# Kernel tuning notes

Measured on AMD Instinct MI355X. Metric: run time of the kernel, lower is better.

Reference implementation:

```python
import jax, jax.numpy as jnp
import numpy as np

THRESHOLD = 0.5
TEMPERATURE = 4.0
LOG_CLAMP = -100.0  # torch BCELoss clamps log terms at -100

B, C, K = 131072, 128, 64


def setup_inputs() -> dict:
    key = jax.random.key(0)
    k1, k2, k3, k4, k5 = jax.random.split(key, 5)
    # sigmoid-like probabilities in (0, 1)
    output = jax.random.uniform(k1, (B, C), dtype=jnp.float32)
    output_consistency = jax.random.uniform(k2, (B, C), dtype=jnp.float32)
    label = jax.random.uniform(k3, (B, C), dtype=jnp.float32)
    class_idx = jnp.sort(jax.random.randint(k4, (K,), 0, C)).astype(jnp.int64)
    batch_mask = jax.random.randint(k5, (B,), 0, 2).astype(bool)
    return {
        "output": output,
        "output_consistency": output_consistency,
        "label": label,
        "class_idx": class_idx,
        "batch_mask": batch_mask,
    }


def _clamped_log(x):
    return jnp.maximum(jnp.log(x), LOG_CLAMP)


def reference(output, output_consistency, label, class_idx, batch_mask):
    # gather the class columns of interest: [B, K]
    o = output[:, class_idx]
    oc = output_consistency[:, class_idx]
    y = label[:, class_idx]

    # sharpened pseudo-label (branch on threshold, fused via where)
    sharp = jnp.where(o > THRESHOLD,
                      o + (1.0 - o) / TEMPERATURE,
                      o - o / TEMPERATURE)

    # per-element BCE (torch BCELoss semantics with log clamp)
    bce = -(y * _clamped_log(o) + (1.0 - y) * _clamped_log(1.0 - o))
    pseudo = (o - sharp) ** 2          # F.mse_loss on scalars
    consistency = (oc - sharp) ** 2

    per_elem = bce + pseudo + consistency            # [B, K]
    row_mask = batch_mask.astype(per_elem.dtype)     # [B]
    total = jnp.sum(per_elem * row_mask[:, None])
    cnt = jnp.sum(row_mask) * per_elem.shape[1]
    return total / cnt
```

## Files before the change

### kernel.cpp

```cpp
#include <hip/hip_runtime.h>

#define BLOCK  256
#define B_ROWS 131072
#define C_COLS 128
#define K_SEL  64
#define TOTAL_VEC (B_ROWS * C_COLS / 4)
#define GRID (TOTAL_VEC / BLOCK)


__global__ __launch_bounds__(BLOCK) void semi_loss_main(
    const float* __restrict__ out,
    const float* __restrict__ outc,
    const float* __restrict__ lab,
    const int*  __restrict__ class_idx,
    const int*  __restrict__ batch_mask,
    float2* __restrict__ partials)
{
    __shared__ float w[C_COLS];
    if (threadIdx.x < C_COLS) w[threadIdx.x] = 0.0f;
    __syncthreads();
    if (threadIdx.x < K_SEL) {
        int c = class_idx[threadIdx.x];
        atomicAdd(&w[c], 1.0f);
    }
    __syncthreads();

    const int v   = blockIdx.x * BLOCK + threadIdx.x;
    const int row = v >> 5;
    const int c4  = v & 31;
    const int col = c4 << 2;

    const int m = batch_mask[row];

    float sum  = 0.0f;
    float cntf = (c4 == 0 && m) ? 1.0f : 0.0f;

    if (m) {
        float4 o4  = ((const float4*)out )[v];
        float4 oc4 = ((const float4*)outc)[v];
        float4 y4  = ((const float4*)lab )[v];

        float ov[4]  = {o4.x,  o4.y,  o4.z,  o4.w};
        float ocv[4] = {oc4.x, oc4.y, oc4.z, oc4.w};
        float yv[4]  = {y4.x,  y4.y,  y4.z,  y4.w};

        #pragma unroll
        for (int j = 0; j < 4; ++j) {
            float wc = w[col + j];
            float o  = ov[j];
            float oc = ocv[j];
            float y  = yv[j];

            float sharp = (o > 0.5f) ? (o + (1.0f - o) * 0.25f)
                                     : (o - o * 0.25f);
            float lo  = fmaxf(logf(o),        -100.0f);
            float l1o = fmaxf(logf(1.0f - o), -100.0f);
            float bce = -(y * lo + (1.0f - y) * l1o);

            float dp = o  - sharp;
            float dc = oc - sharp;
            sum += wc * (bce + dp * dp + dc * dc);
        }
    }

    #pragma unroll
    for (int off = 32; off > 0; off >>= 1) {
        sum  += __shfl_down(sum,  off);
        cntf += __shfl_down(cntf, off);
    }
    __shared__ float ssum[BLOCK / 64];
    __shared__ float scnt[BLOCK / 64];
    int wave = threadIdx.x >> 6;
    int lane = threadIdx.x & 63;
    if (lane == 0) { ssum[wave] = sum; scnt[wave] = cntf; }
    __syncthreads();
    if (threadIdx.x == 0) {
        float s = 0.0f, c = 0.0f;
        #pragma unroll
        for (int i = 0; i < BLOCK / 64; ++i) { s += ssum[i]; c += scnt[i]; }
        partials[blockIdx.x] = make_float2(s, c);
    }
}

__global__ __launch_bounds__(BLOCK) void semi_loss_reduce(
    const float2* __restrict__ partials, float* __restrict__ out)
{
    double s = 0.0, c = 0.0;
    for (int i = threadIdx.x; i < GRID; i += BLOCK) {
        float2 p = partials[i];
        s += (double)p.x;
        c += (double)p.y;
    }
    #pragma unroll
    for (int off = 32; off > 0; off >>= 1) {
        s += __shfl_down(s, off);
        c += __shfl_down(c, off);
    }
    __shared__ double dsum[BLOCK / 64];
    __shared__ double dcnt[BLOCK / 64];
    int wave = threadIdx.x >> 6;
    int lane = threadIdx.x & 63;
    if (lane == 0) { dsum[wave] = s; dcnt[wave] = c; }
    __syncthreads();
    if (threadIdx.x == 0) {
        double ts = 0.0, tc = 0.0;
        #pragma unroll
        for (int i = 0; i < BLOCK / 64; ++i) { ts += dsum[i]; tc += dcnt[i]; }
        out[0] = (float)(ts / (tc * (double)K_SEL));
    }
}

extern "C" void kernel_launch(void* const* d_in, const int* in_sizes, int n_in,
                              void* d_out, int out_size, void* d_ws, size_t ws_size,
                              hipStream_t stream) {
    const float* out_p  = (const float*)d_in[0];
    const float* outc_p = (const float*)d_in[1];
    const float* lab_p  = (const float*)d_in[2];
    const int*   cidx_p = (const int*)d_in[3];
    const int*   mask_p = (const int*)d_in[4];
    float2* partials = (float2*)d_ws;

    semi_loss_main<<<GRID, BLOCK, 0, stream>>>(out_p, outc_p, lab_p,
                                               cidx_p, mask_p, partials);
    semi_loss_reduce<<<1, BLOCK, 0, stream>>>(partials, (float*)d_out);
}
```

Measured before the change: 194.4 us.

## Precompute class weights, process two vectors per thread, use fast log

Builds the per-column class-weight table once in a tiny kernel instead of per block with LDS atomics and barriers. Each thread now handles two float4 vectors, issues all loads unconditionally and masks the result arithmetically, and uses the hardware log2 intrinsic. This removes per-block setup and the load dependency on the mask. In exchange it reads masked rows that were previously skipped, adds a kernel launch, and accepts reduced log accuracy.

```diff
diff --git a/kernel.cpp b/kernel.cpp
--- a/kernel.cpp
+++ b/kernel.cpp
@@ -1,67 +1,80 @@
 #include <hip/hip_runtime.h>
 
-#define BLOCK  256
-#define B_ROWS 131072
-#define C_COLS 128
-#define K_SEL  64
+#define BLOCK   256
+#define B_ROWS  131072
+#define C_COLS  128
+#define K_SEL   64
 #define TOTAL_VEC (B_ROWS * C_COLS / 4)
-#define GRID (TOTAL_VEC / BLOCK)
+#define NTHREADS  (TOTAL_VEC / 2)
+#define GRID      (NTHREADS / BLOCK)
 
+#define WS_PARTIALS_OFF 1024
+
+__global__ void build_w(const int* __restrict__ class_idx,
+                        float* __restrict__ w)
+{
+    int c = threadIdx.x;
+    int cnt = 0;
+    #pragma unroll
+    for (int k = 0; k < K_SEL; ++k)
+        cnt += (class_idx[k] == c) ? 1 : 0;
+    w[c] = (float)cnt;
+}
+
+__device__ __forceinline__ float fast_log(float x) {
+    return __log2f(x) * 0.6931471805599453f;
+}
+
+__device__ __forceinline__ float per_elem_loss(float o, float oc, float y,
+                                               float wc) {
+    float sharp = (o > 0.5f) ? (o + (1.0f - o) * 0.25f)
+                             : (o - o * 0.25f);
+    float lo  = fmaxf(fast_log(o),        -100.0f);
+    float l1o = fmaxf(fast_log(1.0f - o), -100.0f);
+    float bce = -(y * lo + (1.0f - y) * l1o);
+    float dp = o  - sharp;
+    float dc = oc - sharp;
+    return wc * (bce + dp * dp + dc * dc);
+}
 
 __global__ __launch_bounds__(BLOCK) void semi_loss_main(
     const float* __restrict__ out,
     const float* __restrict__ outc,
     const float* __restrict__ lab,
-    const int*  __restrict__ class_idx,
     const int*  __restrict__ batch_mask,
+    const float* __restrict__ wtab,
     float2* __restrict__ partials)
 {
-    __shared__ float w[C_COLS];
-    if (threadIdx.x < C_COLS) w[threadIdx.x] = 0.0f;
-    __syncthreads();
-    if (threadIdx.x < K_SEL) {
-        int c = class_idx[threadIdx.x];
-        atomicAdd(&w[c], 1.0f);
-    }
-    __syncthreads();
+    const int tid = blockIdx.x * BLOCK + threadIdx.x;
+    const int v0  = tid;
+    const int v1  = tid + NTHREADS;
+    const int c4  = v0 & 31;
 
-    const int v   = blockIdx.x * BLOCK + threadIdx.x;
-    const int row = v >> 5;
-    const int c4  = v & 31;
-    const int col = c4 << 2;
+    const int m0 = batch_mask[v0 >> 5];
+    const int m1 = batch_mask[v1 >> 5];
+    const float4 w4  = ((const float4*)wtab)[c4];
 
-    const int m = batch_mask[row];
+    const float4 o0  = ((const float4*)out )[v0];
+    const float4 oc0 = ((const float4*)outc)[v0];
+    const float4 y0  = ((const float4*)lab )[v0];
+    const float4 o1  = ((const float4*)out )[v1];
+    const float4 oc1 = ((const float4*)outc)[v1];
+    const float4 y1  = ((const float4*)lab )[v1];
 
-    float sum  = 0.0f;
-    float cntf = (c4 == 0 && m) ? 1.0f : 0.0f;
+    const float mf0 = m0 ? 1.0f : 0.0f;
+    const float mf1 = m1 ? 1.0f : 0.0f;
 
-    if (m) {
-        float4 o4  = ((const float4*)out )[v];
-        float4 oc4 = ((const float4*)outc)[v];
-        float4 y4  = ((const float4*)lab )[v];
+    float s0 = per_elem_loss(o0.x, oc0.x, y0.x, w4.x)
+             + per_elem_loss(o0.y, oc0.y, y0.y, w4.y)
+             + per_elem_loss(o0.z, oc0.z, y0.z, w4.z)
+             + per_elem_loss(o0.w, oc0.w, y0.w, w4.w);
+    float s1 = per_elem_loss(o1.x, oc1.x, y1.x, w4.x)
+             + per_elem_loss(o1.y, oc1.y, y1.y, w4.y)
+             + per_elem_loss(o1.z, oc1.z, y1.z, w4.z)
+             + per_elem_loss(o1.w, oc1.w, y1.w, w4.w);
 
-        float ov[4]  = {o4.x,  o4.y,  o4.z,  o4.w};
-        float ocv[4] = {oc4.x, oc4.y, oc4.z, oc4.w};
-        float yv[4]  = {y4.x,  y4.y,  y4.z,  y4.w};
-
-        #pragma unroll
-        for (int j = 0; j < 4; ++j) {
-            float wc = w[col + j];
-            float o  = ov[j];
-            float oc = ocv[j];
-            float y  = yv[j];
-
-            float sharp = (o > 0.5f) ? (o + (1.0f - o) * 0.25f)
-                                     : (o - o * 0.25f);
-            float lo  = fmaxf(logf(o),        -100.0f);
-            float l1o = fmaxf(logf(1.0f - o), -100.0f);
-            float bce = -(y * lo + (1.0f - y) * l1o);
-
-            float dp = o  - sharp;
-            float dc = oc - sharp;
-            sum += wc * (bce + dp * dp + dc * dc);
-        }
-    }
+    float sum  = mf0 * s0 + mf1 * s1;
+    float cntf = (c4 == 0) ? (mf0 + mf1) : 0.0f;
 
     #pragma unroll
     for (int off = 32; off > 0; off >>= 1) {
@@ -118,9 +131,12 @@
     const float* lab_p  = (const float*)d_in[2];
     const int*   cidx_p = (const int*)d_in[3];
     const int*   mask_p = (const int*)d_in[4];
-    float2* partials = (float2*)d_ws;
 
+    float*  wtab     = (float*)d_ws;
+    float2* partials = (float2*)((char*)d_ws + WS_PARTIALS_OFF);
+
+    build_w<<<1, C_COLS, 0, stream>>>(cidx_p, wtab);
     semi_loss_main<<<GRID, BLOCK, 0, stream>>>(out_p, outc_p, lab_p,
-                                               cidx_p, mask_p, partials);
+                                               mask_p, wtab, partials);
     semi_loss_reduce<<<1, BLOCK, 0, stream>>>(partials, (float*)d_out);
 }
```

Measured after the change: 207.8 us. 1.07x slower.
